# Kernel optimization log

Hardware: AMD Instinct MI355X
Metric: run time of the kernel (lower is better)

Reference implementation:

```python
import jax, jax.numpy as jnp
import numpy as np

N_NODES = 50000
N_EDGES = 800000
HID = 256
OUT = 128
NEG_SLOPE = 0.2


def gat_layer(x, src, dst, W_src, W_dst, a_src_vec, a_dst_vec, bias, n_nodes):
    # Dense projections (PyG lin_src / lin_dst for tuple in_channels)
    h_src = x @ W_src              # [N, C]
    h_dst = x @ W_dst              # [N, C]
    # Per-node attention logits (att_src/att_dst dot products)
    a_src = h_src @ a_src_vec      # [N]
    a_dst = h_dst @ a_dst_vec      # [N]
    # Edge logits + LeakyReLU
    e = jax.nn.leaky_relu(a_src[src] + a_dst[dst], NEG_SLOPE)  # [E]
    # Segment softmax over incoming edges of each dst node
    m = jax.ops.segment_max(e, dst, num_segments=n_nodes)      # [N]
    m = jnp.where(jnp.isfinite(m), m, 0.0)                      # empty segments
    ex = jnp.exp(e - m[dst])                                    # [E]
    s = jax.ops.segment_sum(ex, dst, num_segments=n_nodes)     # [N]
    alpha = ex / (s[dst] + 1e-16)                               # [E]
    # Attention-weighted message aggregation (scatter-add to dst)
    msg = alpha[:, None] * h_src[src]                           # [E, C]
    out = jax.ops.segment_sum(msg, dst, num_segments=n_nodes)  # [N, C]
    return out + bias


def setup_inputs() -> dict:
    key = jax.random.key(0)
    ks = jax.random.split(key, 12)
    x = jax.random.normal(ks[0], (N_NODES, HID), dtype=jnp.float32)
    edge_index = jax.random.randint(ks[1], (2, N_EDGES), 0, N_NODES, dtype=jnp.int64)
    sc1 = 1.0 / np.sqrt(HID)
    sc2 = 1.0 / np.sqrt(HID)
    return {
        "x": x,
        "edge_index": edge_index,
        "W1_src": jax.random.normal(ks[2], (HID, HID), dtype=jnp.float32) * sc1,
        "W1_dst": jax.random.normal(ks[3], (HID, HID), dtype=jnp.float32) * sc1,
        "att1_src": jax.random.normal(ks[4], (HID,), dtype=jnp.float32) * sc1,
        "att1_dst": jax.random.normal(ks[5], (HID,), dtype=jnp.float32) * sc1,
        "b1": jnp.zeros((HID,), dtype=jnp.float32),
        "W2_src": jax.random.normal(ks[6], (HID, OUT), dtype=jnp.float32) * sc2,
        "W2_dst": jax.random.normal(ks[7], (HID, OUT), dtype=jnp.float32) * sc2,
        "att2_src": jax.random.normal(ks[8], (OUT,), dtype=jnp.float32) * (1.0 / np.sqrt(OUT)),
        "att2_dst": jax.random.normal(ks[9], (OUT,), dtype=jnp.float32) * (1.0 / np.sqrt(OUT)),
        "b2": jnp.zeros((OUT,), dtype=jnp.float32),
    }


def reference(x, edge_index, W1_src, W1_dst, att1_src, att1_dst, b1,
              W2_src, W2_dst, att2_src, att2_dst, b2):
    src, dst = edge_index[0], edge_index[1]
    h = gat_layer(x, src, dst, W1_src, W1_dst, att1_src, att1_dst, b1, N_NODES)
    h = jax.nn.relu(h)
    out = gat_layer(h, src, dst, W2_src, W2_dst, att2_src, att2_dst, b2, N_NODES)
    return out
```

## Files before the change

kernel.cpp:

```cpp
#include <hip/hip_runtime.h>
#include <math.h>

#define N_NODES 50000
#define N_EDGES 800000
#define HID 256
#define OUT_C 128
#define NEG_SLOPE 0.2f
#define SCAN_NB ((N_NODES + 255) / 256)

typedef __attribute__((ext_vector_type(8))) short bf16x8;
typedef __attribute__((ext_vector_type(4))) float f32x4;
typedef _Float16 half_t;
typedef __attribute__((ext_vector_type(4))) _Float16 half4;
typedef __attribute__((ext_vector_type(2))) _Float16 half2t;

__device__ inline unsigned short bf16_rne(float x) {
    unsigned u = __float_as_uint(x);
    return (unsigned short)((u + 0x7fffu + ((u >> 16) & 1u)) >> 16);
}

__device__ __forceinline__ void async_copy16(const void* g, void* l) {
    __builtin_amdgcn_global_load_lds(
        (const __attribute__((address_space(1))) unsigned int*)g,
        (__attribute__((address_space(3))) unsigned int*)l, 16, 0, 0);
}


__global__ __launch_bounds__(256) void hist_rank_kernel(
    const int* __restrict__ dst, int* __restrict__ counts, int* __restrict__ rank) {
    int e = blockIdx.x * 256 + threadIdx.x;
    if (e < N_EDGES) rank[e] = atomicAdd(&counts[dst[e]], 1);
}

__global__ __launch_bounds__(256) void block_scan_kernel(
    const int* __restrict__ counts, int* __restrict__ excl,
    int* __restrict__ blockSums, int n) {
    __shared__ int waveSums[4];
    int i = blockIdx.x * 256 + threadIdx.x;
    int lane = threadIdx.x & 63;
    int wv = threadIdx.x >> 6;
    int c = (i < n) ? counts[i] : 0;
    int v = c;
    #pragma unroll
    for (int off = 1; off < 64; off <<= 1) {
        int t = __shfl_up(v, off);
        if (lane >= off) v += t;
    }
    if (lane == 63) waveSums[wv] = v;
    __syncthreads();
    int waveOff = 0;
    #pragma unroll
    for (int w = 0; w < 4; w++)
        if (w < wv) waveOff += waveSums[w];
    if (i < n) excl[i] = waveOff + v - c;
    if (threadIdx.x == 255) blockSums[blockIdx.x] = waveOff + v;
}

__global__ __launch_bounds__(256) void add_offsets_kernel(
    int* __restrict__ excl, const int* __restrict__ blockSums, int n) {
    __shared__ int lds[4];
    int tid = threadIdx.x;
    int partial = 0;
    for (int j = tid; j < (int)blockIdx.x; j += 256) partial += blockSums[j];
    #pragma unroll
    for (int off = 32; off > 0; off >>= 1) partial += __shfl_down(partial, off);
    if ((tid & 63) == 0) lds[tid >> 6] = partial;
    __syncthreads();
    int prefix = lds[0] + lds[1] + lds[2] + lds[3];
    int i = blockIdx.x * 256 + tid;
    if (i < n) excl[i] += prefix;
    if (i == 0) excl[n] = N_EDGES;
}


#define PACK1_T (8 * 17 * 64)
#define PACK2_T (8 * 9 * 64)
#define EDGE_BLOCKS ((N_EDGES + 255) / 256)
#define PACK_BLOCKS ((PACK1_T + PACK2_T + 255) / 256)
#define V_BLOCKS 128

__global__ __launch_bounds__(256) void prep_kernel(
    const int* __restrict__ src, const int* __restrict__ dst,
    const int* __restrict__ offsets, const int* __restrict__ rank,
    int* __restrict__ src_sorted,
    const float* __restrict__ W1s, const float* __restrict__ att1s,
    const float* __restrict__ W1d, const float* __restrict__ att1d,
    const float* __restrict__ W2s, const float* __restrict__ att2s,
    const float* __restrict__ W2d, const float* __restrict__ att2d,
    unsigned short* __restrict__ hi1, unsigned short* __restrict__ lo1,
    unsigned short* __restrict__ hi2, unsigned short* __restrict__ lo2) {
    if (blockIdx.x < EDGE_BLOCKS) {
        int e = blockIdx.x * 256 + threadIdx.x;
        if (e < N_EDGES)
            src_sorted[offsets[dst[e]] + rank[e]] = src[e];
        return;
    }
    if (blockIdx.x < EDGE_BLOCKS + PACK_BLOCKS) {
        int t = (blockIdx.x - EDGE_BLOCKS) * 256 + threadIdx.x;
        const float *W; unsigned short *hi, *lo; int cout, NTL, tt;
        if (t < PACK1_T)            { tt = t;           W = W1s; hi = hi1; lo = lo1; cout = HID;  NTL = 17; }
        else if (t < PACK1_T + PACK2_T) { tt = t - PACK1_T; W = W2s; hi = hi2; lo = lo2; cout = OUT_C; NTL = 9; }
        else return;
        int lane = tt & 63;
        int tile = (tt >> 6) % NTL;
        if (tile == NTL - 1) return;
        int ks = tt / (64 * NTL);
        int m = lane & 15;
        int kbase = ks * 32 + (lane >> 4) * 8;
        #pragma unroll
        for (int j = 0; j < 8; j++) {
            float val = W[(size_t)(kbase + j) * cout + tile * 16 + m];
            unsigned short h = bf16_rne(val);
            hi[tt * 8 + j] = h;
            lo[tt * 8 + j] = bf16_rne(val - __uint_as_float((unsigned)h << 16));
        }
        return;
    }
    int vb = blockIdx.x - EDGE_BLOCKS - PACK_BLOCKS;
    int layer = vb >> 6;
    int wave = threadIdx.x >> 6, lane = threadIdx.x & 63;
    int k = (vb & 63) * 4 + wave;
    const float *Ws, *Wd, *as_, *ad_; unsigned short *hi, *lo; int cout, NTL;
    if (layer == 0) { Ws = W1s; Wd = W1d; as_ = att1s; ad_ = att1d; hi = hi1; lo = lo1; cout = HID;  NTL = 17; }
    else            { Ws = W2s; Wd = W2d; as_ = att2s; ad_ = att2d; hi = hi2; lo = lo2; cout = OUT_C; NTL = 9; }
    float vs = 0.f, vd = 0.f;
    for (int j = lane; j < cout; j += 64) {
        vs += Ws[(size_t)k * cout + j] * as_[j];
        vd += Wd[(size_t)k * cout + j] * ad_[j];
    }
    #pragma unroll
    for (int off = 32; off > 0; off >>= 1) {
        vs += __shfl_down(vs, off);
        vd += __shfl_down(vd, off);
    }
    vs = __shfl(vs, 0);
    vd = __shfl(vd, 0);
    int ks = k >> 5, quad = (k >> 3) & 3, j = k & 7;
    if (lane < 32) {
        int m = lane & 15;
        int tt = ks * 64 * NTL + (NTL - 1) * 64 + quad * 16 + m;
        float val = (m == 0) ? vs : (m == 1) ? vd : 0.f;
        unsigned short h = bf16_rne(val);
        if (lane < 16) hi[tt * 8 + j] = h;
        else           lo[tt * 8 + j] = bf16_rne(val - __uint_as_float((unsigned)h << 16));
    }
}


template <int COUT, int NT, int RG, bool WRITE_A, bool ASPLIT>
__device__ __forceinline__ void gemm_body(
    const float* __restrict__ A,
    const unsigned short* __restrict__ Ahi, const unsigned short* __restrict__ Alo,
    const unsigned short* __restrict__ Bhi, const unsigned short* __restrict__ Blo,
    half_t* __restrict__ H,
    float* __restrict__ a_s, float* __restrict__ a_d, int M, int tile0,
    short* sBh, short* sBl) {
    const int NTL = COUT / 16 + 1;
    int wave = threadIdx.x >> 6, lane = threadIdx.x & 63;
    int m = lane & 15, quad = lane >> 4;
    int row0 = blockIdx.x * (RG * 64) + wave * (RG * 16);
    f32x4 acc[RG][NT];
    #pragma unroll
    for (int rg = 0; rg < RG; rg++)
        #pragma unroll
        for (int nt = 0; nt < NT; nt++)
            acc[rg][nt] = (f32x4){0.f, 0.f, 0.f, 0.f};

    const float* arow[RG];
    const unsigned short* arh[RG];
    const unsigned short* arl[RG];
    #pragma unroll
    for (int rg = 0; rg < RG; rg++) {
        int r = row0 + rg * 16 + m;
        if (r >= M) r = M - 1;
        if (ASPLIT) {
            arh[rg] = Ahi + (size_t)r * HID;
            arl[rg] = Alo + (size_t)r * HID;
        } else {
            arow[rg] = A + (size_t)r * HID;
        }
    }

    auto STAGE = [&](int ks, int b) {
        for (int u = wave; u < 2 * NT; u += 4) {
            int nt = (u < NT) ? u : u - NT;
            int tile = (WRITE_A && nt == NT - 1) ? (COUT / 16) : (tile0 + nt);
            size_t goff = ((size_t)(ks * NTL + tile) * 64 + lane) * 8;
            if (u < NT) async_copy16(Bhi + goff, sBh + b * NT * 512 + nt * 512);
            else        async_copy16(Blo + goff, sBl + b * NT * 512 + nt * 512);
        }
    };

    STAGE(0, 0);
    __syncthreads();
    int cur = 0;
    for (int ks = 0; ks < 8; ks++) {
        if (ks < 7) STAGE(ks + 1, cur ^ 1);

        bf16x8 ah[RG], al[RG];
        #pragma unroll
        for (int rg = 0; rg < RG; rg++) {
            if (ASPLIT) {
                ah[rg] = *(const bf16x8*)(arh[rg] + ks * 32 + quad * 8);
                al[rg] = *(const bf16x8*)(arl[rg] + ks * 32 + quad * 8);
            } else {
                const float* ap = arow[rg] + ks * 32 + quad * 8;
                float4 v0 = *(const float4*)ap;
                float4 v1 = *(const float4*)(ap + 4);
                float av[8] = {v0.x, v0.y, v0.z, v0.w, v1.x, v1.y, v1.z, v1.w};
                #pragma unroll
                for (int j = 0; j < 8; j++) {
                    unsigned short h = bf16_rne(av[j]);
                    float hf = __uint_as_float((unsigned)h << 16);
                    ah[rg][j] = (short)h;
                    al[rg][j] = (short)bf16_rne(av[j] - hf);
                }
            }
        }
        #pragma unroll
        for (int nt = 0; nt < NT; nt++) {
            bf16x8 bh = *(const bf16x8*)(sBh + cur * NT * 512 + nt * 512 + lane * 8);
            bf16x8 bl = *(const bf16x8*)(sBl + cur * NT * 512 + nt * 512 + lane * 8);
            #pragma unroll
            for (int rg = 0; rg < RG; rg++) {
                acc[rg][nt] = __builtin_amdgcn_mfma_f32_16x16x32_bf16(ah[rg], bh, acc[rg][nt], 0, 0, 0);
                acc[rg][nt] = __builtin_amdgcn_mfma_f32_16x16x32_bf16(ah[rg], bl, acc[rg][nt], 0, 0, 0);
                acc[rg][nt] = __builtin_amdgcn_mfma_f32_16x16x32_bf16(al[rg], bh, acc[rg][nt], 0, 0, 0);
            }
        }
        __syncthreads();
        cur ^= 1;
    }
    const int NW = WRITE_A ? NT - 1 : NT;
    #pragma unroll
    for (int rg = 0; rg < RG; rg++)
        #pragma unroll
        for (int nt = 0; nt < NW; nt++)
            #pragma unroll
            for (int r = 0; r < 4; r++) {
                int row = row0 + rg * 16 + quad * 4 + r;
                if (row < M)
                    H[(size_t)row * COUT + (tile0 + nt) * 16 + m] = (half_t)acc[rg][nt][r];
            }
    if (WRITE_A) {
        #pragma unroll
        for (int rg = 0; rg < RG; rg++)
            #pragma unroll
            for (int r = 0; r < 4; r++) {
                int row = row0 + rg * 16 + quad * 4 + r;
                if (row < M) {
                    if (m == 0) a_s[row] = acc[rg][NT - 1][r];
                    else if (m == 1) a_d[row] = acc[rg][NT - 1][r];
                }
            }
    }
}

template <int COUT, int RG, bool ASPLIT>
__global__ __launch_bounds__(256) void mfma_gemm_a_kernel(
    const float* __restrict__ A,
    const unsigned short* __restrict__ Ahi, const unsigned short* __restrict__ Alo,
    const unsigned short* __restrict__ Bhi, const unsigned short* __restrict__ Blo,
    half_t* __restrict__ H,
    float* __restrict__ a_s, float* __restrict__ a_d, int M) {
    __shared__ short sBh[2 * 9 * 512];
    __shared__ short sBl[2 * 9 * 512];
    if (blockIdx.y == 0)
        gemm_body<COUT, 9, RG, true, ASPLIT>(A, Ahi, Alo, Bhi, Blo, H, a_s, a_d, M, 0, sBh, sBl);
    else
        gemm_body<COUT, 8, RG, false, ASPLIT>(A, Ahi, Alo, Bhi, Blo, H, a_s, a_d, M, 8, sBh, sBl);
}


template <int C, bool RELU, bool OSPLIT>
__global__ __launch_bounds__(256) void fused_aggregate_kernel(
    const int* __restrict__ offsets, const int* __restrict__ src_sorted,
    const float* __restrict__ a_src, const float* __restrict__ a_dst,
    const half_t* __restrict__ h, const float* __restrict__ bias,
    float* __restrict__ out,
    unsigned short* __restrict__ outhi, unsigned short* __restrict__ outlo) {
    constexpr int CH = 8;
    int node = (int)((blockIdx.x * 256u + threadIdx.x) >> 6);
    int lane = threadIdx.x & 63;
    if (node >= N_NODES) return;
    int beg = offsets[node], end = offsets[node + 1];
    float ad = a_dst[node];
    float s = 0.f;

    if (C == 256) {
        float4 acc = make_float4(0.f, 0.f, 0.f, 0.f);
        for (int base = beg; base < end; base += CH) {
            int cnt = end - base; if (cnt > CH) cnt = CH;
            int idx[CH];
            #pragma unroll
            for (int j = 0; j < CH; j++)
                idx[j] = src_sorted[(j < cnt) ? base + j : base];
            half4 hv[CH];
            #pragma unroll
            for (int j = 0; j < CH; j++)
                hv[j] = *(const half4*)(h + ((unsigned)idx[j] * C + lane * 4));
            float w[CH];
            #pragma unroll
            for (int j = 0; j < CH; j++) {
                float l = a_src[idx[j]] + ad;
                l = fmaxf(l, l * NEG_SLOPE);
                w[j] = (j < cnt) ? __expf(l) : 0.f;
                s += w[j];
            }
            #pragma unroll
            for (int j = 0; j < CH; j++) {
                acc.x += w[j] * (float)hv[j][0]; acc.y += w[j] * (float)hv[j][1];
                acc.z += w[j] * (float)hv[j][2]; acc.w += w[j] * (float)hv[j][3];
            }
        }
        float inv = 1.f / (s + 1e-16f);
        float4 bv = *(const float4*)(bias + lane * 4);
        acc.x = acc.x * inv + bv.x; acc.y = acc.y * inv + bv.y;
        acc.z = acc.z * inv + bv.z; acc.w = acc.w * inv + bv.w;
        if (RELU) {
            acc.x = fmaxf(acc.x, 0.f); acc.y = fmaxf(acc.y, 0.f);
            acc.z = fmaxf(acc.z, 0.f); acc.w = fmaxf(acc.w, 0.f);
        }
        if (OSPLIT) {
            float o[4] = {acc.x, acc.y, acc.z, acc.w};
            ushort4 h4, l4;
            unsigned short* hp = (unsigned short*)&h4;
            unsigned short* lp = (unsigned short*)&l4;
            #pragma unroll
            for (int j = 0; j < 4; j++) {
                unsigned short hh = bf16_rne(o[j]);
                hp[j] = hh;
                lp[j] = bf16_rne(o[j] - __uint_as_float((unsigned)hh << 16));
            }
            *(ushort4*)(outhi + (size_t)node * C + lane * 4) = h4;
            *(ushort4*)(outlo + (size_t)node * C + lane * 4) = l4;
        } else {
            *(float4*)(out + (size_t)node * C + lane * 4) = acc;
        }
    } else {
        float2 acc = make_float2(0.f, 0.f);
        for (int base = beg; base < end; base += CH) {
            int cnt = end - base; if (cnt > CH) cnt = CH;
            int idx[CH];
            #pragma unroll
            for (int j = 0; j < CH; j++)
                idx[j] = src_sorted[(j < cnt) ? base + j : base];
            half2t hv[CH];
            #pragma unroll
            for (int j = 0; j < CH; j++)
                hv[j] = *(const half2t*)(h + ((unsigned)idx[j] * C + lane * 2));
            float w[CH];
            #pragma unroll
            for (int j = 0; j < CH; j++) {
                float l = a_src[idx[j]] + ad;
                l = fmaxf(l, l * NEG_SLOPE);
                w[j] = (j < cnt) ? __expf(l) : 0.f;
                s += w[j];
            }
            #pragma unroll
            for (int j = 0; j < CH; j++) {
                acc.x += w[j] * (float)hv[j][0]; acc.y += w[j] * (float)hv[j][1];
            }
        }
        float inv = 1.f / (s + 1e-16f);
        float2 bv = *(const float2*)(bias + lane * 2);
        acc.x = acc.x * inv + bv.x; acc.y = acc.y * inv + bv.y;
        if (RELU) { acc.x = fmaxf(acc.x, 0.f); acc.y = fmaxf(acc.y, 0.f); }
        *(float2*)(out + (size_t)node * C + lane * 2) = acc;
    }
}

extern "C" void kernel_launch(void* const* d_in, const int* in_sizes, int n_in,
                              void* d_out, int out_size, void* d_ws, size_t ws_size,
                              hipStream_t stream) {
    const float* x     = (const float*)d_in[0];
    const int*   edge  = (const int*)d_in[1];
    const int*   src   = edge;
    const int*   dst   = edge + N_EDGES;
    const float* W1s   = (const float*)d_in[2];
    const float* W1d   = (const float*)d_in[3];
    const float* att1s = (const float*)d_in[4];
    const float* att1d = (const float*)d_in[5];
    const float* b1    = (const float*)d_in[6];
    const float* W2s   = (const float*)d_in[7];
    const float* W2d   = (const float*)d_in[8];
    const float* att2s = (const float*)d_in[9];
    const float* att2d = (const float*)d_in[10];
    const float* b2    = (const float*)d_in[11];
    float* out = (float*)d_out;

    float* ws    = (float*)d_ws;
    half_t* h1   = (half_t*)ws;
    unsigned short* act2hi = (unsigned short*)(ws + (size_t)N_NODES * HID);
    unsigned short* act2lo = act2hi + (size_t)N_NODES * HID;
    float* a_s   = ws + 2 * (size_t)N_NODES * HID;
    float* a_d   = a_s + N_NODES;
    int* ibase      = (int*)(a_d + N_NODES);
    int* src_sorted = ibase;
    int* rank       = src_sorted + N_EDGES;
    int* counts     = rank + N_EDGES;
    int* offsets    = counts + N_NODES;
    int* blockSums  = offsets + N_NODES + 1;
    unsigned short* wp1h = (unsigned short*)(((uintptr_t)(blockSums + SCAN_NB) + 15) & ~(uintptr_t)15);
    unsigned short* wp1l = wp1h + PACK1_T * 8;
    unsigned short* wp2h = wp1l + PACK1_T * 8;
    unsigned short* wp2l = wp2h + PACK2_T * 8;
    half_t* h2 = h1;

    const int waveBlocksN = (N_NODES + 3) / 4;
    const int gemmBlocks1 = (N_NODES + 127) / 128;
    const int gemmBlocks2 = (N_NODES + 63) / 64;

    hipMemsetAsync(counts, 0, N_NODES * sizeof(int), stream);
    hist_rank_kernel<<<EDGE_BLOCKS, 256, 0, stream>>>(dst, counts, rank);
    block_scan_kernel<<<SCAN_NB, 256, 0, stream>>>(counts, offsets, blockSums, N_NODES);
    add_offsets_kernel<<<SCAN_NB, 256, 0, stream>>>(offsets, blockSums, N_NODES);

    prep_kernel<<<EDGE_BLOCKS + PACK_BLOCKS + V_BLOCKS, 256, 0, stream>>>(
        src, dst, offsets, rank, src_sorted,
        W1s, att1s, W1d, att1d, W2s, att2s, W2d, att2d,
        wp1h, wp1l, wp2h, wp2l);

    mfma_gemm_a_kernel<HID, 2, false><<<dim3(gemmBlocks1, 2), 256, 0, stream>>>(
        x, nullptr, nullptr, wp1h, wp1l, h1, a_s, a_d, N_NODES);
    fused_aggregate_kernel<HID, true, true><<<waveBlocksN, 256, 0, stream>>>(
        offsets, src_sorted, a_s, a_d, h1, b1, nullptr, act2hi, act2lo);

    mfma_gemm_a_kernel<OUT_C, 1, true><<<dim3(gemmBlocks2, 1), 256, 0, stream>>>(
        nullptr, act2hi, act2lo, wp2h, wp2l, h2, a_s, a_d, N_NODES);
    fused_aggregate_kernel<OUT_C, false, false><<<waveBlocksN, 256, 0, stream>>>(
        offsets, src_sorted, a_s, a_d, h2, b2, out, nullptr, nullptr);
}
```

Measured before the change: 304.9 us.

## Prefetch next A tile in GEMM and fuse histogram with weight packing

```diff
diff --git a/kernel.cpp b/kernel.cpp
--- a/kernel.cpp
+++ b/kernel.cpp
@@ -25,64 +25,15 @@
         (__attribute__((address_space(3))) unsigned int*)l, 16, 0, 0);
 }
 
-
-__global__ __launch_bounds__(256) void hist_rank_kernel(
-    const int* __restrict__ dst, int* __restrict__ counts, int* __restrict__ rank) {
-    int e = blockIdx.x * 256 + threadIdx.x;
-    if (e < N_EDGES) rank[e] = atomicAdd(&counts[dst[e]], 1);
-}
-
-__global__ __launch_bounds__(256) void block_scan_kernel(
-    const int* __restrict__ counts, int* __restrict__ excl,
-    int* __restrict__ blockSums, int n) {
-    __shared__ int waveSums[4];
-    int i = blockIdx.x * 256 + threadIdx.x;
-    int lane = threadIdx.x & 63;
-    int wv = threadIdx.x >> 6;
-    int c = (i < n) ? counts[i] : 0;
-    int v = c;
-    #pragma unroll
-    for (int off = 1; off < 64; off <<= 1) {
-        int t = __shfl_up(v, off);
-        if (lane >= off) v += t;
-    }
-    if (lane == 63) waveSums[wv] = v;
-    __syncthreads();
-    int waveOff = 0;
-    #pragma unroll
-    for (int w = 0; w < 4; w++)
-        if (w < wv) waveOff += waveSums[w];
-    if (i < n) excl[i] = waveOff + v - c;
-    if (threadIdx.x == 255) blockSums[blockIdx.x] = waveOff + v;
-}
-
-__global__ __launch_bounds__(256) void add_offsets_kernel(
-    int* __restrict__ excl, const int* __restrict__ blockSums, int n) {
-    __shared__ int lds[4];
-    int tid = threadIdx.x;
-    int partial = 0;
-    for (int j = tid; j < (int)blockIdx.x; j += 256) partial += blockSums[j];
-    #pragma unroll
-    for (int off = 32; off > 0; off >>= 1) partial += __shfl_down(partial, off);
-    if ((tid & 63) == 0) lds[tid >> 6] = partial;
-    __syncthreads();
-    int prefix = lds[0] + lds[1] + lds[2] + lds[3];
-    int i = blockIdx.x * 256 + tid;
-    if (i < n) excl[i] += prefix;
-    if (i == 0) excl[n] = N_EDGES;
-}
-
-
 #define PACK1_T (8 * 17 * 64)
 #define PACK2_T (8 * 9 * 64)
 #define EDGE_BLOCKS ((N_EDGES + 255) / 256)
 #define PACK_BLOCKS ((PACK1_T + PACK2_T + 255) / 256)
 #define V_BLOCKS 128
 
-__global__ __launch_bounds__(256) void prep_kernel(
-    const int* __restrict__ src, const int* __restrict__ dst,
-    const int* __restrict__ offsets, const int* __restrict__ rank,
-    int* __restrict__ src_sorted,
+
+__global__ __launch_bounds__(256) void hist_prep_kernel(
+    const int* __restrict__ dst, int* __restrict__ counts, int* __restrict__ rank,
     const float* __restrict__ W1s, const float* __restrict__ att1s,
     const float* __restrict__ W1d, const float* __restrict__ att1d,
     const float* __restrict__ W2s, const float* __restrict__ att2s,
@@ -91,8 +42,7 @@
     unsigned short* __restrict__ hi2, unsigned short* __restrict__ lo2) {
     if (blockIdx.x < EDGE_BLOCKS) {
         int e = blockIdx.x * 256 + threadIdx.x;
-        if (e < N_EDGES)
-            src_sorted[offsets[dst[e]] + rank[e]] = src[e];
+        if (e < N_EDGES) rank[e] = atomicAdd(&counts[dst[e]], 1);
         return;
     }
     if (blockIdx.x < EDGE_BLOCKS + PACK_BLOCKS) {
@@ -147,6 +97,56 @@
 }
 
 
+__global__ __launch_bounds__(256) void block_scan_kernel(
+    const int* __restrict__ counts, int* __restrict__ excl,
+    int* __restrict__ blockSums, int n) {
+    __shared__ int waveSums[4];
+    int i = blockIdx.x * 256 + threadIdx.x;
+    int lane = threadIdx.x & 63;
+    int wv = threadIdx.x >> 6;
+    int c = (i < n) ? counts[i] : 0;
+    int v = c;
+    #pragma unroll
+    for (int off = 1; off < 64; off <<= 1) {
+        int t = __shfl_up(v, off);
+        if (lane >= off) v += t;
+    }
+    if (lane == 63) waveSums[wv] = v;
+    __syncthreads();
+    int waveOff = 0;
+    #pragma unroll
+    for (int w = 0; w < 4; w++)
+        if (w < wv) waveOff += waveSums[w];
+    if (i < n) excl[i] = waveOff + v - c;
+    if (threadIdx.x == 255) blockSums[blockIdx.x] = waveOff + v;
+}
+
+__global__ __launch_bounds__(256) void add_offsets_kernel(
+    int* __restrict__ excl, const int* __restrict__ blockSums, int n) {
+    __shared__ int lds[4];
+    int tid = threadIdx.x;
+    int partial = 0;
+    for (int j = tid; j < (int)blockIdx.x; j += 256) partial += blockSums[j];
+    #pragma unroll
+    for (int off = 32; off > 0; off >>= 1) partial += __shfl_down(partial, off);
+    if ((tid & 63) == 0) lds[tid >> 6] = partial;
+    __syncthreads();
+    int prefix = lds[0] + lds[1] + lds[2] + lds[3];
+    int i = blockIdx.x * 256 + tid;
+    if (i < n) excl[i] += prefix;
+    if (i == 0) excl[n] = N_EDGES;
+}
+
+__global__ __launch_bounds__(256) void scatter_kernel(
+    const int* __restrict__ src, const int* __restrict__ dst,
+    const int* __restrict__ offsets, const int* __restrict__ rank,
+    int* __restrict__ src_sorted) {
+    int e = blockIdx.x * 256 + threadIdx.x;
+    if (e >= N_EDGES) return;
+    src_sorted[offsets[dst[e]] + rank[e]] = src[e];
+}
+
+
 template <int COUT, int NT, int RG, bool WRITE_A, bool ASPLIT>
 __device__ __forceinline__ void gemm_body(
     const float* __restrict__ A,
@@ -191,29 +191,43 @@
         }
     };
 
+    bf16x8 ahc[RG], alc[RG];
+    #pragma unroll
+    for (int rg = 0; rg < RG; rg++) {
+        if (ASPLIT) {
+            ahc[rg] = *(const bf16x8*)(arh[rg] + quad * 8);
+            alc[rg] = *(const bf16x8*)(arl[rg] + quad * 8);
+        } else {
+            const float* ap = arow[rg] + quad * 8;
+            float4 v0 = *(const float4*)ap;
+            float4 v1 = *(const float4*)(ap + 4);
+            float av[8] = {v0.x, v0.y, v0.z, v0.w, v1.x, v1.y, v1.z, v1.w};
+            #pragma unroll
+            for (int j = 0; j < 8; j++) {
+                unsigned short h = bf16_rne(av[j]);
+                ahc[rg][j] = (short)h;
+                alc[rg][j] = (short)bf16_rne(av[j] - __uint_as_float((unsigned)h << 16));
+            }
+        }
+    }
+
     STAGE(0, 0);
     __syncthreads();
     int cur = 0;
     for (int ks = 0; ks < 8; ks++) {
-        if (ks < 7) STAGE(ks + 1, cur ^ 1);
-
-        bf16x8 ah[RG], al[RG];
-        #pragma unroll
-        for (int rg = 0; rg < RG; rg++) {
-            if (ASPLIT) {
-                ah[rg] = *(const bf16x8*)(arh[rg] + ks * 32 + quad * 8);
-                al[rg] = *(const bf16x8*)(arl[rg] + ks * 32 + quad * 8);
-            } else {
-                const float* ap = arow[rg] + ks * 32 + quad * 8;
-                float4 v0 = *(const float4*)ap;
-                float4 v1 = *(const float4*)(ap + 4);
-                float av[8] = {v0.x, v0.y, v0.z, v0.w, v1.x, v1.y, v1.z, v1.w};
-                #pragma unroll
-                for (int j = 0; j < 8; j++) {
-                    unsigned short h = bf16_rne(av[j]);
-                    float hf = __uint_as_float((unsigned)h << 16);
-                    ah[rg][j] = (short)h;
-                    al[rg][j] = (short)bf16_rne(av[j] - hf);
+        float4 a0n[RG], a1n[RG];
+        bf16x8 ahn[RG], aln[RG];
+        if (ks < 7) {
+            STAGE(ks + 1, cur ^ 1);
+            #pragma unroll
+            for (int rg = 0; rg < RG; rg++) {
+                if (ASPLIT) {
+                    ahn[rg] = *(const bf16x8*)(arh[rg] + (ks + 1) * 32 + quad * 8);
+                    aln[rg] = *(const bf16x8*)(arl[rg] + (ks + 1) * 32 + quad * 8);
+                } else {
+                    const float* ap = arow[rg] + (ks + 1) * 32 + quad * 8;
+                    a0n[rg] = *(const float4*)ap;
+                    a1n[rg] = *(const float4*)(ap + 4);
                 }
             }
         }
@@ -223,9 +237,27 @@
             bf16x8 bl = *(const bf16x8*)(sBl + cur * NT * 512 + nt * 512 + lane * 8);
             #pragma unroll
             for (int rg = 0; rg < RG; rg++) {
-                acc[rg][nt] = __builtin_amdgcn_mfma_f32_16x16x32_bf16(ah[rg], bh, acc[rg][nt], 0, 0, 0);
-                acc[rg][nt] = __builtin_amdgcn_mfma_f32_16x16x32_bf16(ah[rg], bl, acc[rg][nt], 0, 0, 0);
-                acc[rg][nt] = __builtin_amdgcn_mfma_f32_16x16x32_bf16(al[rg], bh, acc[rg][nt], 0, 0, 0);
+                acc[rg][nt] = __builtin_amdgcn_mfma_f32_16x16x32_bf16(ahc[rg], bh, acc[rg][nt], 0, 0, 0);
+                acc[rg][nt] = __builtin_amdgcn_mfma_f32_16x16x32_bf16(ahc[rg], bl, acc[rg][nt], 0, 0, 0);
+                acc[rg][nt] = __builtin_amdgcn_mfma_f32_16x16x32_bf16(alc[rg], bh, acc[rg][nt], 0, 0, 0);
+            }
+        }
+        if (ks < 7) {
+            #pragma unroll
+            for (int rg = 0; rg < RG; rg++) {
+                if (ASPLIT) {
+                    ahc[rg] = ahn[rg];
+                    alc[rg] = aln[rg];
+                } else {
+                    float av[8] = {a0n[rg].x, a0n[rg].y, a0n[rg].z, a0n[rg].w,
+                                   a1n[rg].x, a1n[rg].y, a1n[rg].z, a1n[rg].w};
+                    #pragma unroll
+                    for (int j = 0; j < 8; j++) {
+                        unsigned short h = bf16_rne(av[j]);
+                        ahc[rg][j] = (short)h;
+                        alc[rg][j] = (short)bf16_rne(av[j] - __uint_as_float((unsigned)h << 16));
+                    }
+                }
             }
         }
         __syncthreads();
@@ -412,14 +444,13 @@
     const int gemmBlocks2 = (N_NODES + 63) / 64;
 
     hipMemsetAsync(counts, 0, N_NODES * sizeof(int), stream);
-    hist_rank_kernel<<<EDGE_BLOCKS, 256, 0, stream>>>(dst, counts, rank);
+    hist_prep_kernel<<<EDGE_BLOCKS + PACK_BLOCKS + V_BLOCKS, 256, 0, stream>>>(
+        dst, counts, rank,
+        W1s, att1s, W1d, att1d, W2s, att2s, W2d, att2d,
+        wp1h, wp1l, wp2h, wp2l);
     block_scan_kernel<<<SCAN_NB, 256, 0, stream>>>(counts, offsets, blockSums, N_NODES);
     add_offsets_kernel<<<SCAN_NB, 256, 0, stream>>>(offsets, blockSums, N_NODES);
-
-    prep_kernel<<<EDGE_BLOCKS + PACK_BLOCKS + V_BLOCKS, 256, 0, stream>>>(
-        src, dst, offsets, rank, src_sorted,
-        W1s, att1s, W1d, att1d, W2s, att2s, W2d, att2d,
-        wp1h, wp1l, wp2h, wp2l);
+    scatter_kernel<<<EDGE_BLOCKS, 256, 0, stream>>>(src, dst, offsets, rank, src_sorted);
 
     mfma_gemm_a_kernel<HID, 2, false><<<dim3(gemmBlocks1, 2), 256, 0, stream>>>(
         x, nullptr, nullptr, wp1h, wp1l, h1, a_s, a_d, N_NODES);
```

New measurement: 305.5 us. No clear change (+0.2%).
